# Kernel optimization log

Hardware: AMD Instinct MI355X
Metric: run time of the kernel (lower is better)

## Reference

```python
import jax, jax.numpy as jnp
import numpy as np

B, C, H, W = 8, 512, 64, 64
CDIV = 8
CFG = C // CDIV  # f/g channels = 64


def setup_inputs() -> dict:
    key = jax.random.key(0)
    ks = jax.random.split(key, 8)
    x = jax.random.normal(ks[0], (B, C, H, W), dtype=jnp.float32)
    # 1x1 conv weights (spectral-norm omitted: weights used as-given), orthogonal-ish small init
    Wf = jax.random.normal(ks[1], (CFG, C), dtype=jnp.float32) * 0.02
    bf = jnp.zeros((CFG,), dtype=jnp.float32)
    Wg = jax.random.normal(ks[2], (CFG, C), dtype=jnp.float32) * 0.02
    bg = jnp.zeros((CFG,), dtype=jnp.float32)
    Wh = jax.random.normal(ks[3], (C, C), dtype=jnp.float32) * 0.02
    bh = jnp.zeros((C,), dtype=jnp.float32)
    # module inits gamma=0 (identity output); use 0.5 so the attention path is exercised
    gamma = jnp.float32(0.5)
    return {"x": x, "Wf": Wf, "bf": bf, "Wg": Wg, "bg": bg, "Wh": Wh, "bh": bh, "gamma": gamma}


def reference(x, Wf, bf, Wg, bg, Wh, bh, gamma):
    Bb, Cc, Hh, Ww = x.shape
    N = Hh * Ww
    xf = x.reshape(Bb, Cc, N)  # [B, C, N]
    # 1x1 convs == per-pixel linear maps
    f = jnp.einsum('oc,bcn->bon', Wf, xf) + bf[:, None]  # [B, CFG, N]
    g = jnp.einsum('oc,bcn->bon', Wg, xf) + bg[:, None]  # [B, CFG, N]
    h = jnp.einsum('oc,bcn->bon', Wh, xf) + bh[:, None]  # [B, C, N]
    # attention scores over spatial tokens: queries g, keys f -> [B, N, N]
    s = jnp.einsum('bci,bcj->bij', g, f)
    beta = jax.nn.softmax(s, axis=-1)
    o = jnp.einsum('bij,bcj->bci', beta, h).reshape(Bb, Cc, Hh, Ww)
    return gamma * o + x
```

## Files before the change

### kernel.cpp

```cpp
#include <hip/hip_runtime.h>
#include <hip/hip_bf16.h>

typedef __bf16 bf16;
typedef __attribute__((ext_vector_type(2))) __bf16 bf16x2;
typedef __attribute__((ext_vector_type(4))) __bf16 bf16x4;
typedef __attribute__((ext_vector_type(8))) __bf16 bf16x8;
typedef __attribute__((ext_vector_type(4))) float f32x4;
typedef __attribute__((ext_vector_type(8))) int i32x8;
typedef unsigned char u8;

#define MFMA16x16x32 __builtin_amdgcn_mfma_f32_16x16x32_bf16
#define MFMA_MX(a, b, c, sa, sb) \
    __builtin_amdgcn_mfma_scale_f32_16x16x128_f8f6f4((a), (b), (c), 0, 0, 0, (sa), 0, (sb))

#define NB 8
#define NC 512
#define NN 4096
#define CFG 64

#define XP 520
#define TP 74

#define EXP_OFF 4.5f
#define SCALE_ONE 0x7F7F7F7F

__global__ __launch_bounds__(256) void k_wprep(
    const float* __restrict__ Wf, const float* __restrict__ bfv,
    const float* __restrict__ Wg, const float* __restrict__ bgv,
    const float* __restrict__ Wh,
    bf16* __restrict__ Wfg, bf16* __restrict__ Whb, float* __restrict__ bfg)
{
    int idx = blockIdx.x * 256 + threadIdx.x;
    if (idx < 32768)       Wfg[idx] = (bf16)Wf[idx];
    else if (idx < 65536)  Wfg[idx] = (bf16)Wg[idx - 32768];
    if (idx < 262144)      Whb[idx] = (bf16)Wh[idx];
    if (idx < 64)          bfg[idx] = bfv[idx];
    else if (idx < 128)    bfg[idx] = bgv[idx - 64];
}

__global__ __launch_bounds__(512) void k_fused(
    const float* __restrict__ x, const bf16* __restrict__ Wfg,
    const float* __restrict__ bfg, const bf16* __restrict__ Whb,
    const float* __restrict__ bh,
    bf16* __restrict__ fF, bf16* __restrict__ gF, u8* __restrict__ hT)
{
    __shared__ bf16 X[64 * XP];
    __shared__ bf16 tile[64 * TP];

    int b = blockIdx.x, n0 = blockIdx.y * 64;
    int t = threadIdx.x;

    for (int cc = 0; cc < 8; cc++) {
        int cl = t >> 3, seg = (t & 7) * 8;
        const float* src = x + ((size_t)(b * NC + cc * 64 + cl)) * NN + n0 + seg;
        float4 v0 = ((const float4*)src)[0];
        float4 v1 = ((const float4*)src)[1];
        bf16* tr = &tile[cl * TP + seg];
        *(bf16x2*)(tr + 0) = bf16x2{(bf16)v0.x, (bf16)v0.y};
        *(bf16x2*)(tr + 2) = bf16x2{(bf16)v0.z, (bf16)v0.w};
        *(bf16x2*)(tr + 4) = bf16x2{(bf16)v1.x, (bf16)v1.y};
        *(bf16x2*)(tr + 6) = bf16x2{(bf16)v1.z, (bf16)v1.w};
        __syncthreads();
        int nl = t >> 3, cs = (t & 7) * 8;
        bf16 buf[8];
#pragma unroll
        for (int u = 0; u < 8; u++) buf[u] = tile[(cs + u) * TP + nl];
        *(bf16x8*)&X[nl * XP + cc * 64 + cs] = *(bf16x8*)buf;
        __syncthreads();
    }

    int w = t >> 6, l = t & 63;
    int lr = l & 15, lq = l >> 4;

    {
        const bf16* Ab = Whb + (size_t)(w * 64) * NC;
        f32x4 acc[4][4] = {};
        for (int k0 = 0; k0 < NC; k0 += 32) {
            bf16x8 a[4], bb[4];
#pragma unroll
            for (int fi = 0; fi < 4; fi++)
                a[fi] = *(const bf16x8*)(Ab + (size_t)(fi*16 + lr) * NC + k0 + lq*8);
#pragma unroll
            for (int fj = 0; fj < 4; fj++)
                bb[fj] = *(const bf16x8*)&X[(fj*16 + lr) * XP + k0 + lq*8];
#pragma unroll
            for (int fi = 0; fi < 4; fi++)
#pragma unroll
                for (int fj = 0; fj < 4; fj++)
                    acc[fi][fj] = MFMA16x16x32(a[fi], bb[fj], acc[fi][fj], 0, 0, 0);
        }
#pragma unroll
        for (int fi = 0; fi < 4; fi++)
#pragma unroll
            for (int fj = 0; fj < 4; fj++)
#pragma unroll
                for (int tt = 0; tt < 4; tt++) {
                    int c = w*64 + fi*16 + lq*4 + tt;
                    int j = n0 + fj*16 + lr;
                    float v = acc[fi][fj][tt] + bh[c];
                    size_t tile128 = (size_t)(b*32 + (j >> 7));
                    size_t ctile   = (size_t)(c >> 4);
                    size_t lane    = (size_t)(((j >> 5) & 3)*16 + (c & 15));
                    size_t off     = ((tile128*32 + ctile)*64 + lane)*32 + (size_t)(j & 31);
                    int pk = __builtin_amdgcn_cvt_pk_fp8_f32(v, v, 0, false);
                    hT[off] = (u8)pk;
                }
    }

    {
        const bf16* Bb = Wfg + (size_t)(w * 16) * NC;
        f32x4 acc2[4] = {};
        for (int k0 = 0; k0 < NC; k0 += 32) {
            bf16x8 a[4], bo;
#pragma unroll
            for (int fi = 0; fi < 4; fi++)
                a[fi] = *(const bf16x8*)&X[(fi*16 + lr) * XP + k0 + lq*8];
            bo = *(const bf16x8*)(Bb + (size_t)lr * NC + k0 + lq*8);
#pragma unroll
            for (int fi = 0; fi < 4; fi++)
                acc2[fi] = MFMA16x16x32(a[fi], bo, acc2[fi], 0, 0, 0);
        }
#pragma unroll
        for (int fi = 0; fi < 4; fi++)
#pragma unroll
            for (int tt = 0; tt < 4; tt++) {
                int n = n0 + fi*16 + lq*4 + tt;
                int o = w*16 + lr;
                float v = acc2[fi][tt] + bfg[o];
                int c = o & 63;
                bf16* dst = (o < 64) ? fF : gF;
                int jt16 = n >> 4, nr = n & 15;
                int ks = c >> 5, lqd = (c >> 3) & 3, e = c & 7;
                size_t off = (((size_t)(b*256 + jt16)*2 + ks)*64 + (lqd*16 + nr))*8 + e;
                dst[off] = (bf16)v;
            }
    }
}

__global__ __launch_bounds__(1024, 4) void k_attn(
    const bf16* __restrict__ fF, const bf16* __restrict__ gF,
    const u8* __restrict__ hT, const float* __restrict__ x,
    const float* __restrict__ gammap, float* __restrict__ out)
{
    __shared__ alignas(16) u8 Pl[2][16384];
    __shared__ alignas(16) bf16 fS[2][8192];
    __shared__ float lpart[8][2][16];
    __shared__ alignas(16) float linv[128];

    int b  = blockIdx.x;
    int i0 = blockIdx.y * 128;
    int t = threadIdx.x;
    int w = t >> 6, l = t & 63;
    int lr = l & 15, lq = l >> 4;

    float gamma = *gammap;
    int fi_s = w >> 1;
    int ks_s = w & 1;
    const int sone = SCALE_ONE;

    u8* Pf = &Pl[0][0];

    const bf16* gbase = gF + ((size_t)(b*256 + (i0 >> 4) + fi_s)*2)*512 + (size_t)l*8;
    bf16x8 bg0 = *(const bf16x8*)(gbase);
    bf16x8 bg1 = *(const bf16x8*)(gbase + 512);

    const bf16* fb0 = fF + (size_t)b*256*2*512;
    const u8* hb0 = hT + (size_t)b*2097152 + (size_t)(w*2)*2048 + (size_t)l*32;

    f32x4 oacc[8][2] = {};
    float lsum = 0.f;

#define F_LOAD(q, reg)  { (reg) = *(const bf16x8*)(fb0 + (size_t)(q)*8192 + t*8); }
#define F_WRITE(q, reg) { *(bf16x8*)&fS[(q) & 1][t*8] = (reg); }

#define S_STEP(jn, fbuf, pbuf)                                                 \
    {                                                                          \
        const bf16* fb = &fS[fbuf][((jn) & 1)*4096 + ks_s*2048] + l*8;         \
        bf16x8 af00 = *(const bf16x8*)(fb);                                    \
        bf16x8 af01 = *(const bf16x8*)(fb + 512);                              \
        bf16x8 af10 = *(const bf16x8*)(fb + 1024);                             \
        bf16x8 af11 = *(const bf16x8*)(fb + 1536);                             \
        f32x4 s0 = {}, s1 = {};                                                \
        s0 = MFMA16x16x32(af00, bg0, s0, 0, 0, 0);                             \
        s0 = MFMA16x16x32(af01, bg1, s0, 0, 0, 0);                             \
        s1 = MFMA16x16x32(af10, bg0, s1, 0, 0, 0);                             \
        s1 = MFMA16x16x32(af11, bg1, s1, 0, 0, 0);                             \
        float e00 = __expf(s0[0] - EXP_OFF), e01 = __expf(s0[1] - EXP_OFF);    \
        float e02 = __expf(s0[2] - EXP_OFF), e03 = __expf(s0[3] - EXP_OFF);    \
        float e10 = __expf(s1[0] - EXP_OFF), e11 = __expf(s1[1] - EXP_OFF);    \
        float e12 = __expf(s1[2] - EXP_OFF), e13 = __expf(s1[3] - EXP_OFF);    \
        lsum += (e00 + e01 + e02 + e03) + (e10 + e11 + e12 + e13);             \
        int pk0 = __builtin_amdgcn_cvt_pk_fp8_f32(e00, e01, 0, false);         \
        pk0     = __builtin_amdgcn_cvt_pk_fp8_f32(e02, e03, pk0, true);        \
        int pk1 = __builtin_amdgcn_cvt_pk_fp8_f32(e10, e11, 0, false);         \
        pk1     = __builtin_amdgcn_cvt_pk_fp8_f32(e12, e13, pk1, true);        \
        u8* pw = Pf + (pbuf)*16384 + fi_s*2048                                 \
                 + ((((jn) & 1)*2 + ks_s)*16 + lr)*32 + lq*4;                  \
        *(int*)(pw)      = pk0;                                                \
        *(int*)(pw + 16) = pk1;                                                \
    }

#define PV_STEP(ph, pbuf)                                                      \
    {                                                                          \
        const u8* hb = hb0 + (size_t)(ph)*65536;                               \
        i32x8 ah0 = *(const i32x8*)(hb);                                       \
        i32x8 ah1 = *(const i32x8*)(hb + 2048);                                \
        const u8* Pr = Pf + (pbuf)*16384 + l*32;                               \
        __builtin_amdgcn_s_setprio(1);                                         \
        _Pragma("unroll")                                                      \
        for (int fi = 0; fi < 8; fi++) {                                       \
            i32x8 ap = *(const i32x8*)(Pr + fi*2048);                          \
            oacc[fi][0] = MFMA_MX(ap, ah0, oacc[fi][0], sone, sone);           \
            oacc[fi][1] = MFMA_MX(ap, ah1, oacc[fi][1], sone, sone);           \
        }                                                                      \
        __builtin_amdgcn_s_setprio(0);                                         \
    }

    {
        bf16x8 fr;
        F_LOAD(0, fr)
        F_WRITE(0, fr)
        __syncthreads();
        F_LOAD(1, fr)
        S_STEP(0, 0, 0)
        S_STEP(1, 0, 0)
        F_WRITE(1, fr)
        __syncthreads();
    }

    for (int p = 0; p < 30; p++) {
        int cur = p & 1, nxt = cur ^ 1;

        bf16x8 fr;
        F_LOAD(p + 2, fr)

        PV_STEP(p, cur)

        S_STEP(2*p + 2, nxt, nxt)
        S_STEP(2*p + 3, nxt, nxt)

        F_WRITE(p + 2, fr)

        __syncthreads();
    }

    PV_STEP(30, 0)
    S_STEP(62, 1, 1)
    S_STEP(63, 1, 1)
    __syncthreads();
    PV_STEP(31, 1)

#undef S_STEP
#undef PV_STEP
#undef F_LOAD
#undef F_WRITE

    lsum += __shfl_xor(lsum, 16, 64);
    lsum += __shfl_xor(lsum, 32, 64);
    if (lq == 0) lpart[fi_s][ks_s][lr] = lsum;
    __syncthreads();
    if (t < 128) {
        linv[t] = 1.0f / (lpart[t >> 4][0][t & 15] + lpart[t >> 4][1][t & 15]);
    }
    __syncthreads();

    int cw = w * 32;
    const float* xb = x + (size_t)b * NC * NN;
    float* ob = out + (size_t)b * NC * NN;
#pragma unroll
    for (int fi = 0; fi < 8; fi++) {
        f32x4 li = *(const f32x4*)&linv[fi*16 + lq*4];
#pragma unroll
        for (int fc = 0; fc < 2; fc++) {
            int c = cw + fc*16 + lr;
            size_t base = (size_t)c * NN + i0 + fi*16 + lq*4;
            float4 xv = *(const float4*)(xb + base);
            float4 ov;
            ov.x = gamma * oacc[fi][fc][0] * li[0] + xv.x;
            ov.y = gamma * oacc[fi][fc][1] * li[1] + xv.y;
            ov.z = gamma * oacc[fi][fc][2] * li[2] + xv.z;
            ov.w = gamma * oacc[fi][fc][3] * li[3] + xv.w;
            *(float4*)(ob + base) = ov;
        }
    }
}

extern "C" void kernel_launch(void* const* d_in, const int* in_sizes, int n_in,
                              void* d_out, int out_size, void* d_ws, size_t ws_size,
                              hipStream_t stream)
{
    const float* x     = (const float*)d_in[0];
    const float* Wf    = (const float*)d_in[1];
    const float* bf_   = (const float*)d_in[2];
    const float* Wg    = (const float*)d_in[3];
    const float* bg_   = (const float*)d_in[4];
    const float* Wh    = (const float*)d_in[5];
    const float* bh_   = (const float*)d_in[6];
    const float* gamma = (const float*)d_in[7];
    float* out = (float*)d_out;

    char* ws = (char*)d_ws;
    u8*    hT  = (u8*)(ws + 33554432);
    bf16*  fF  = (bf16*)(ws + 67108864);
    bf16*  gF  = (bf16*)(ws + 71303168);
    bf16*  Wfg = (bf16*)(ws + 75497472);
    bf16*  Whb = (bf16*)(ws + 75628544);
    float* bfg = (float*)(ws + 76152832);

    k_wprep<<<dim3(1024), dim3(256), 0, stream>>>(Wf, bf_, Wg, bg_, Wh, Wfg, Whb, bfg);
    k_fused<<<dim3(8, 64), dim3(512), 0, stream>>>(x, Wfg, bfg, Whb, bh_, fF, gF, hT);
    k_attn<<<dim3(8, 32), dim3(1024), 0, stream>>>(fF, gF, hT, x, gamma, out);
}
```

Baseline: 174.8 us.

## Split fp8 H and P tiles into 16-byte halves for packed stores and conflict-free loads

The fp8 H projection epilogue swaps the MFMA operands so that each lane holds four consecutive spatial positions. It then writes one packed 32-bit word instead of four single-byte stores. The H and P tile layouts are split into two 1024-byte halves of 16 bytes per lane. PV loads become pairs of 128-bit reads concatenated into the 256-bit MFMA operand. The aim is fewer scattered byte stores and reduced LDS bank conflicts on the P tile, at the cost of extra load instructions.

```diff
diff --git a/kernel.cpp b/kernel.cpp
--- a/kernel.cpp
+++ b/kernel.cpp
@@ -6,12 +6,15 @@
 typedef __attribute__((ext_vector_type(4))) __bf16 bf16x4;
 typedef __attribute__((ext_vector_type(8))) __bf16 bf16x8;
 typedef __attribute__((ext_vector_type(4))) float f32x4;
+typedef __attribute__((ext_vector_type(4))) int i32x4;
 typedef __attribute__((ext_vector_type(8))) int i32x8;
 typedef unsigned char u8;
 
 #define MFMA16x16x32 __builtin_amdgcn_mfma_f32_16x16x32_bf16
 #define MFMA_MX(a, b, c, sa, sb) \
     __builtin_amdgcn_mfma_scale_f32_16x16x128_f8f6f4((a), (b), (c), 0, 0, 0, (sa), 0, (sb))
+
+#define CAT8(lo, hi) (i32x8){(lo)[0], (lo)[1], (lo)[2], (lo)[3], (hi)[0], (hi)[1], (hi)[2], (hi)[3]}
 
 #define NB 8
 #define NC 512
@@ -87,24 +90,29 @@
             for (int fi = 0; fi < 4; fi++)
 #pragma unroll
                 for (int fj = 0; fj < 4; fj++)
-                    acc[fi][fj] = MFMA16x16x32(a[fi], bb[fj], acc[fi][fj], 0, 0, 0);
+                    acc[fi][fj] = MFMA16x16x32(bb[fj], a[fi], acc[fi][fj], 0, 0, 0);
         }
 #pragma unroll
-        for (int fi = 0; fi < 4; fi++)
-#pragma unroll
-            for (int fj = 0; fj < 4; fj++)
-#pragma unroll
-                for (int tt = 0; tt < 4; tt++) {
-                    int c = w*64 + fi*16 + lq*4 + tt;
-                    int j = n0 + fj*16 + lr;
-                    float v = acc[fi][fj][tt] + bh[c];
-                    size_t tile128 = (size_t)(b*32 + (j >> 7));
-                    size_t ctile   = (size_t)(c >> 4);
-                    size_t lane    = (size_t)(((j >> 5) & 3)*16 + (c & 15));
-                    size_t off     = ((tile128*32 + ctile)*64 + lane)*32 + (size_t)(j & 31);
-                    int pk = __builtin_amdgcn_cvt_pk_fp8_f32(v, v, 0, false);
-                    hT[off] = (u8)pk;
-                }
+        for (int fi = 0; fi < 4; fi++) {
+            int c = w*64 + fi*16 + lr;
+            float bias = bh[c];
+            size_t ctile = (size_t)(c >> 4);
+#pragma unroll
+            for (int fj = 0; fj < 4; fj++) {
+                int j0 = n0 + fj*16 + lq*4;
+                float v0 = acc[fi][fj][0] + bias;
+                float v1 = acc[fi][fj][1] + bias;
+                float v2 = acc[fi][fj][2] + bias;
+                float v3 = acc[fi][fj][3] + bias;
+                int pk = __builtin_amdgcn_cvt_pk_fp8_f32(v0, v1, 0, false);
+                pk     = __builtin_amdgcn_cvt_pk_fp8_f32(v2, v3, pk, true);
+                size_t tile128 = (size_t)(b*32) + (size_t)(j0 >> 7);
+                size_t hk   = (size_t)((j0 >> 4) & 1);
+                size_t lane = (size_t)(((j0 >> 5) & 3)*16 + (c & 15));
+                size_t off = ((tile128*32 + ctile)*2 + hk)*1024 + lane*16 + (size_t)(j0 & 15);
+                *(int*)(hT + off) = pk;
+            }
+        }
     }
 
     {
@@ -165,7 +173,7 @@
     bf16x8 bg1 = *(const bf16x8*)(gbase + 512);
 
     const bf16* fb0 = fF + (size_t)b*256*2*512;
-    const u8* hb0 = hT + (size_t)b*2097152 + (size_t)(w*2)*2048 + (size_t)l*32;
+    const u8* hb0 = hT + (size_t)b*2097152 + (size_t)(w*2)*2048 + (size_t)l*16;
 
     f32x4 oacc[8][2] = {};
     float lsum = 0.f;
@@ -195,21 +203,27 @@
         int pk1 = __builtin_amdgcn_cvt_pk_fp8_f32(e10, e11, 0, false);         \
         pk1     = __builtin_amdgcn_cvt_pk_fp8_f32(e12, e13, pk1, true);        \
         u8* pw = Pf + (pbuf)*16384 + fi_s*2048                                 \
-                 + ((((jn) & 1)*2 + ks_s)*16 + lr)*32 + lq*4;                  \
-        *(int*)(pw)      = pk0;                                                \
-        *(int*)(pw + 16) = pk1;                                                \
+                 + ((((jn) & 1)*2 + ks_s)*16 + lr)*16 + lq*4;                  \
+        *(int*)(pw)        = pk0;                                              \
+        *(int*)(pw + 1024) = pk1;                                              \
     }
 
 #define PV_STEP(ph, pbuf)                                                      \
     {                                                                          \
         const u8* hb = hb0 + (size_t)(ph)*65536;                               \
-        i32x8 ah0 = *(const i32x8*)(hb);                                       \
-        i32x8 ah1 = *(const i32x8*)(hb + 2048);                                \
-        const u8* Pr = Pf + (pbuf)*16384 + l*32;                               \
+        i32x4 hl0 = *(const i32x4*)(hb);                                       \
+        i32x4 hh0 = *(const i32x4*)(hb + 1024);                                \
+        i32x4 hl1 = *(const i32x4*)(hb + 2048);                                \
+        i32x4 hh1 = *(const i32x4*)(hb + 3072);                                \
+        i32x8 ah0 = CAT8(hl0, hh0);                                            \
+        i32x8 ah1 = CAT8(hl1, hh1);                                            \
+        const u8* Pr = Pf + (pbuf)*16384 + l*16;                               \
         __builtin_amdgcn_s_setprio(1);                                         \
         _Pragma("unroll")                                                      \
         for (int fi = 0; fi < 8; fi++) {                                       \
-            i32x8 ap = *(const i32x8*)(Pr + fi*2048);                          \
+            i32x4 plo = *(const i32x4*)(Pr + fi*2048);                         \
+            i32x4 phi = *(const i32x4*)(Pr + fi*2048 + 1024);                  \
+            i32x8 ap = CAT8(plo, phi);                                         \
             oacc[fi][0] = MFMA_MX(ap, ah0, oacc[fi][0], sone, sone);           \
             oacc[fi][1] = MFMA_MX(ap, ah1, oacc[fi][1], sone, sone);           \
         }                                                                      \
```

New measurement: 165.5 us (median of 2 runs). -5.4%, faster.
